# Optimization experiments

Measured on AMD Instinct MI355X. Metric: run time of the kernel, lower is better.

Reference implementation:

```python
import jax, jax.numpy as jnp
from jax import lax
import numpy as np

B, A, D = 4, 512, 729   # batch, num_angles, detector pixels
H, W = 512, 512         # reconstruction volume


def setup_inputs() -> dict:
    key = jax.random.key(0)
    sino = jax.random.normal(key, (B, A, D), dtype=jnp.float32)
    vol_spacing = np.array([1.0, 1.0], dtype=np.float32)          # (sy, sx)
    det_spacing = np.array([1.0], dtype=np.float32)
    vol_origin = np.array([-(H - 1) / 2.0, -(W - 1) / 2.0], dtype=np.float32)
    det_origin = np.array([-(D - 1) / 2.0], dtype=np.float32)
    angles = jnp.linspace(0.0, jnp.pi, A, endpoint=False, dtype=jnp.float32)
    return {
        "input": sino,
        "volume_shape": np.array([H, W], dtype=np.int64),
        "volume_origin": jnp.asarray(vol_origin),
        "detector_origin": jnp.asarray(det_origin),
        "volume_spacing": jnpp if False else jnp.asarray(vol_spacing),
        "detector_spacing": jnp.asarray(det_spacing),
        "trajectory": angles,
    }


def _backproject(sino, vol_shape, vol_origin, det_origin, vol_spacing, det_spacing, angles):
    h, w = int(vol_shape[0]), int(vol_shape[1])
    d = sino.shape[-1]
    ys = vol_origin[0] + jnp.arange(h, dtype=sino.dtype) * vol_spacing[0]  # [H]
    xs = vol_origin[1] + jnp.arange(w, dtype=sino.dtype) * vol_spacing[1]  # [W]

    def step(acc, per_angle):
        theta, sino_a = per_angle                      # scalar, [B, D]
        # ray coordinate s = x*cos(theta) + y*sin(theta) for every voxel
        s = xs[None, :] * jnp.cos(theta) + ys[:, None] * jnp.sin(theta)  # [H, W]
        u = (s - det_origin[0]) / det_spacing[0]       # continuous detector index
        u0 = jnp.floor(u)
        frac = u - u0
        i0 = u0.astype(jnp.int32)
        i1 = i0 + 1
        valid0 = (i0 >= 0) & (i0 < d)
        valid1 = (i1 >= 0) & (i1 < d)
        i0c = jnp.clip(i0, 0, d - 1)
        i1c = jnp.clip(i1, 0, d - 1)
        v0 = sino_a[:, i0c]                            # [B, H, W] gather
        v1 = sino_a[:, i1c]                            # [B, H, W] gather
        contrib = (jnp.where(valid0, (1.0 - frac) * v0, 0.0)
                   + jnp.where(valid1, frac * v1, 0.0))
        return acc + contrib, None

    acc0 = jnp.zeros((sino.shape[0], h, w), dtype=sino.dtype)
    out, _ = lax.scan(step, acc0, (angles, jnp.swapaxes(sino, 0, 1)))
    return out


def reference(input, volume_shape, volume_origin, detector_origin,
              volume_spacing, detector_spacing, trajectory):
    return _backproject(input, volume_shape, volume_origin, detector_origin,
                        volume_spacing, detector_spacing, trajectory)
```

## Files before the change

kernel.cpp:

```cpp
#include <hip/hip_runtime.h>

#define BB 4
#define AA 512
#define ZS 8
#define AH (AA / ZS)
#define DD 729
#define HH 512
#define WW 512
#define CH 4
#define NC (AH / CH)
#define WIN 32

typedef float f4v __attribute__((ext_vector_type(4)));

__device__ inline void gload_lds(const float* g, float* l) {
    __builtin_amdgcn_global_load_lds(
        (const __attribute__((address_space(1))) unsigned int*)g,
        (__attribute__((address_space(3))) unsigned int*)l, 4, 0, 0);
}

#define WAIT_VM8 0x0F78
#define WAIT_VM0 0x0F70

__global__ __launch_bounds__(64, 8) void bp_kernel(
    const float* __restrict__ sino,
    const float* __restrict__ vol_origin,
    const float* __restrict__ det_origin,
    const float* __restrict__ vol_spacing,
    const float* __restrict__ det_spacing,
    const float* __restrict__ angles,
    float* __restrict__ out)
{
    __shared__ f4v   s_csk[AH];
    __shared__ int   s_s0[AH];
    __shared__ float s_win[2][CH * WIN * BB];

    const int lane = threadIdx.y * 16 + threadIdx.x;

    const float inv_ds = 1.0f / det_spacing[0];
    const int abase = blockIdx.z * AH;

    const int x0 = blockIdx.x * 16;
    const int y0 = blockIdx.y * 16;
    const float vsx = vol_spacing[1], vsy = vol_spacing[0];
    const float off = -det_origin[0] * inv_ds;
    const float xc = vol_origin[1] + ((float)x0 + 7.5f) * vsx;
    const float yc = vol_origin[0] + ((float)y0 + 7.5f) * vsy;

    {
        const int a = lane;
        float th = angles[abase + a];
        float c = cosf(th) * inv_ds;
        float s = sinf(th) * inv_ds;
        float uc = fmaf(xc, c, fmaf(yc, s, off));
        int s0 = min(max((int)uc - (WIN / 2), 0), DD - WIN);
        f4v k;
        k.x = c; k.y = s; k.z = off - (float)s0; k.w = 4.0f * vsy * s;
        s_csk[a] = k;
        s_s0[a]  = s0;
    }
    __builtin_amdgcn_s_waitcnt(0xC070);

    const int ix  = x0 + threadIdx.x;
    const int iy0 = y0 + threadIdx.y;
    const float xw = vol_origin[1] + (float)ix * vsx;
    const float yw = vol_origin[0] + (float)iy0 * vsy;

    const long sg0 = (long)(lane & 3) * (AA * DD) + (lane >> 2);

    f4v acc0 = {0.f, 0.f, 0.f, 0.f};
    f4v acc1 = {0.f, 0.f, 0.f, 0.f};
    f4v acc2 = {0.f, 0.f, 0.f, 0.f};
    f4v acc3 = {0.f, 0.f, 0.f, 0.f};

    #define STAGE(C, P)                                                    \
        do {                                                               \
            _Pragma("unroll")                                              \
            for (int i = 0; i < CH; ++i) {                                 \
                const int  aa  = (C) * CH + i;                             \
                const long row = (long)(abase + aa) * DD + s_s0[aa];       \
                float* dst = &s_win[P][i * (WIN * BB)];                    \
                gload_lds(sino + row + sg0, dst);                          \
                gload_lds(sino + row + sg0 + 16, dst + 64);                \
            }                                                              \
        } while (0)

    #define LERP(U, ACC)                                                   \
        do {                                                               \
            const int   li = (int)(U);                                     \
            const float fr = __builtin_amdgcn_fractf(U);                   \
            const float om = 1.0f - fr;                                    \
            const f4v* w = (const f4v*)&s_win[p][(j * WIN + li) * BB];     \
            const f4v P = w[0], Q = w[1];                                  \
            const f4v fr4 = {fr, fr, fr, fr};                              \
            const f4v om4 = {om, om, om, om};                              \
            ACC = ACC + fr4 * Q + om4 * P;                                 \
        } while (0)

    int p = 0;
    STAGE(0, 0);
    for (int c = 0; c < NC; ++c) {
        if (c + 1 < NC) {
            STAGE(c + 1, p ^ 1);
            __builtin_amdgcn_s_waitcnt(WAIT_VM8);
        } else {
            __builtin_amdgcn_s_waitcnt(WAIT_VM0);
        }
        #pragma unroll
        for (int j = 0; j < CH; ++j) {
            const f4v  k  = s_csk[c * CH + j];
            const float u0 = fmaf(xw, k.x, fmaf(yw, k.y, k.z));
            const float u1 = u0 + k.w;
            const float u2 = u1 + k.w;
            const float u3 = u2 + k.w;
            LERP(u0, acc0);
            LERP(u1, acc1);
            LERP(u2, acc2);
            LERP(u3, acc3);
        }
        p ^= 1;
    }
    #undef STAGE
    #undef LERP

    const size_t HW = (size_t)HH * WW;
    #define OUT4(ACC, ROWOFF)                                              \
        do {                                                               \
            const size_t o = (size_t)(iy0 + (ROWOFF)) * WW + ix;           \
            unsafeAtomicAdd(&out[o],          (ACC).x);                    \
            unsafeAtomicAdd(&out[o + HW],     (ACC).y);                    \
            unsafeAtomicAdd(&out[o + 2 * HW], (ACC).z);                    \
            unsafeAtomicAdd(&out[o + 3 * HW], (ACC).w);                    \
        } while (0)
    OUT4(acc0, 0);
    OUT4(acc1, 4);
    OUT4(acc2, 8);
    OUT4(acc3, 12);
    #undef OUT4
}

extern "C" void kernel_launch(void* const* d_in, const int* in_sizes, int n_in,
                              void* d_out, int out_size, void* d_ws, size_t ws_size,
                              hipStream_t stream) {
    const float* sino        = (const float*)d_in[0];
    const float* vol_origin  = (const float*)d_in[2];
    const float* det_origin  = (const float*)d_in[3];
    const float* vol_spacing = (const float*)d_in[4];
    const float* det_spacing = (const float*)d_in[5];
    const float* angles      = (const float*)d_in[6];
    float* out = (float*)d_out;

    hipMemsetAsync(d_out, 0, (size_t)out_size * sizeof(float), stream);

    dim3 block(16, 4, 1);
    dim3 grid(WW / 16, HH / 16, ZS);
    bp_kernel<<<grid, block, 0, stream>>>(sino, vol_origin, det_origin,
                                          vol_spacing, det_spacing, angles, out);
}
```

Measured before the change: 139.7 us.

## Stage sinogram windows as packed fp16 and interpolate with half2 FMAs

Replaces the direct global-to-LDS double-buffered staging with buffer loads into registers. The loaded values are converted to packed fp16 pairs and written to a single LDS buffer between two barriers. Interpolation then runs with half2 FMAs, and the fp16 partial sums are widened into fp32 accumulators after every chunk of four angles. This halves LDS footprint and read bandwidth and doubles arithmetic density, but adds two barriers per chunk, conversion work, and fp16 precision loss. It also lowers the occupancy hint in the launch bounds.

```diff
diff --git a/kernel.cpp b/kernel.cpp
--- a/kernel.cpp
+++ b/kernel.cpp
@@ -1,4 +1,5 @@
 #include <hip/hip_runtime.h>
+#include <hip/hip_fp16.h>
 
 #define BB 4
 #define AA 512
@@ -11,18 +12,22 @@
 #define NC (AH / CH)
 #define WIN 32
 
-typedef float f4v __attribute__((ext_vector_type(4)));
+typedef float        f4v  __attribute__((ext_vector_type(4)));
+typedef unsigned int u4v8 __attribute__((ext_vector_type(4), aligned(8)));
 
-__device__ inline void gload_lds(const float* g, float* l) {
-    __builtin_amdgcn_global_load_lds(
-        (const __attribute__((address_space(1))) unsigned int*)g,
-        (__attribute__((address_space(3))) unsigned int*)l, 4, 0, 0);
+__device__ inline float buf_load1(__amdgpu_buffer_rsrc_t r, int elem) {
+    union { unsigned int u; float f; } c;
+    c.u = __builtin_amdgcn_raw_buffer_load_b32(r, elem * 4, 0, 0);
+    return c.f;
+}
+__device__ inline __half2 h2bc(unsigned int x) {
+    return __builtin_bit_cast(__half2, x);
+}
+__device__ inline unsigned int pk2u(float a, float b) {
+    return __builtin_bit_cast(unsigned int, __builtin_amdgcn_cvt_pkrtz(a, b));
 }
 
-#define WAIT_VM8 0x0F78
-#define WAIT_VM0 0x0F70
-
-__global__ __launch_bounds__(64, 8) void bp_kernel(
+__global__ __launch_bounds__(64, 4) void bp_kernel(
     const float* __restrict__ sino,
     const float* __restrict__ vol_origin,
     const float* __restrict__ det_origin,
@@ -31,9 +36,9 @@
     const float* __restrict__ angles,
     float* __restrict__ out)
 {
-    __shared__ f4v   s_csk[AH];
-    __shared__ int   s_s0[AH];
-    __shared__ float s_win[2][CH * WIN * BB];
+    __shared__ f4v          s_csk[AH];
+    __shared__ int          s_s0[AH];
+    __shared__ unsigned int s_win[CH * WIN * 2];
 
     const int lane = threadIdx.y * 16 + threadIdx.x;
 
@@ -59,53 +64,76 @@
         s_csk[a] = k;
         s_s0[a]  = s0;
     }
-    __builtin_amdgcn_s_waitcnt(0xC070);
+    __syncthreads();
 
     const int ix  = x0 + threadIdx.x;
     const int iy0 = y0 + threadIdx.y;
     const float xw = vol_origin[1] + (float)ix * vsx;
     const float yw = vol_origin[0] + (float)iy0 * vsy;
 
-    const long sg0 = (long)(lane & 3) * (AA * DD) + (lane >> 2);
+    const int hh = lane & 1;
+    const int ee = lane >> 1;
+    const int gA = (2 * hh) * (AA * DD) + ee;
+
+    const __amdgpu_buffer_rsrc_t rsrc = __builtin_amdgcn_make_buffer_rsrc(
+        (void*)sino, (short)0, BB * AA * DD * 4, 0x00020000);
 
     f4v acc0 = {0.f, 0.f, 0.f, 0.f};
     f4v acc1 = {0.f, 0.f, 0.f, 0.f};
     f4v acc2 = {0.f, 0.f, 0.f, 0.f};
     f4v acc3 = {0.f, 0.f, 0.f, 0.f};
 
-    #define STAGE(C, P)                                                    \
+    const __half2 hz = h2bc(0u);
+    __half2 h01_0 = hz, h23_0 = hz, h01_1 = hz, h23_1 = hz;
+    __half2 h01_2 = hz, h23_2 = hz, h01_3 = hz, h23_3 = hz;
+
+    float vA0, vB0, vA1, vB1, vA2, vB2, vA3, vB3;
+
+    #define STAGE_LOAD(C)                                                  \
         do {                                                               \
-            _Pragma("unroll")                                              \
-            for (int i = 0; i < CH; ++i) {                                 \
-                const int  aa  = (C) * CH + i;                             \
-                const long row = (long)(abase + aa) * DD + s_s0[aa];       \
-                float* dst = &s_win[P][i * (WIN * BB)];                    \
-                gload_lds(sino + row + sg0, dst);                          \
-                gload_lds(sino + row + sg0 + 16, dst + 64);                \
-            }                                                              \
+            const int aa = (C) * CH;                                       \
+            const int r0 = (abase + aa + 0) * DD + s_s0[aa + 0] + gA;      \
+            const int r1 = (abase + aa + 1) * DD + s_s0[aa + 1] + gA;      \
+            const int r2 = (abase + aa + 2) * DD + s_s0[aa + 2] + gA;      \
+            const int r3 = (abase + aa + 3) * DD + s_s0[aa + 3] + gA;      \
+            vA0 = buf_load1(rsrc, r0); vB0 = buf_load1(rsrc, r0 + AA * DD);\
+            vA1 = buf_load1(rsrc, r1); vB1 = buf_load1(rsrc, r1 + AA * DD);\
+            vA2 = buf_load1(rsrc, r2); vB2 = buf_load1(rsrc, r2 + AA * DD);\
+            vA3 = buf_load1(rsrc, r3); vB3 = buf_load1(rsrc, r3 + AA * DD);\
         } while (0)
 
-    #define LERP(U, ACC)                                                   \
+    #define CONVERT_WRITE()                                                \
+        do {                                                               \
+            s_win[0 * 64 + lane] = pk2u(vA0, vB0);                         \
+            s_win[1 * 64 + lane] = pk2u(vA1, vB1);                         \
+            s_win[2 * 64 + lane] = pk2u(vA2, vB2);                         \
+            s_win[3 * 64 + lane] = pk2u(vA3, vB3);                         \
+        } while (0)
+
+    #define LERP(U, H01, H23)                                              \
         do {                                                               \
             const int   li = (int)(U);                                     \
             const float fr = __builtin_amdgcn_fractf(U);                   \
-            const float om = 1.0f - fr;                                    \
-            const f4v* w = (const f4v*)&s_win[p][(j * WIN + li) * BB];     \
-            const f4v P = w[0], Q = w[1];                                  \
-            const f4v fr4 = {fr, fr, fr, fr};                              \
-            const f4v om4 = {om, om, om, om};                              \
-            ACC = ACC + fr4 * Q + om4 * P;                                 \
+            const __half2 fr2 = h2bc(pk2u(fr, fr));                        \
+            const __half2 om2 = h2bc(pk2u(1.0f - fr, 1.0f - fr));          \
+            const u4v8 t = *(const u4v8*)&s_win[(j * WIN + li) * 2];       \
+            H01 = __hfma2(h2bc(t.x), om2, __hfma2(h2bc(t.z), fr2, H01));   \
+            H23 = __hfma2(h2bc(t.y), om2, __hfma2(h2bc(t.w), fr2, H23));   \
         } while (0)
 
-    int p = 0;
-    STAGE(0, 0);
+    #define WIDEN(H01, H23, ACC)                                           \
+        do {                                                               \
+            (ACC).x += __low2float(H01);  (ACC).y += __high2float(H01);    \
+            (ACC).z += __low2float(H23);  (ACC).w += __high2float(H23);    \
+            H01 = hz; H23 = hz;                                            \
+        } while (0)
+
+    STAGE_LOAD(0);
     for (int c = 0; c < NC; ++c) {
-        if (c + 1 < NC) {
-            STAGE(c + 1, p ^ 1);
-            __builtin_amdgcn_s_waitcnt(WAIT_VM8);
-        } else {
-            __builtin_amdgcn_s_waitcnt(WAIT_VM0);
-        }
+        __syncthreads();
+        CONVERT_WRITE();
+        __syncthreads();
+        if (c + 1 < NC) STAGE_LOAD(c + 1);
         #pragma unroll
         for (int j = 0; j < CH; ++j) {
             const f4v  k  = s_csk[c * CH + j];
@@ -113,15 +141,20 @@
             const float u1 = u0 + k.w;
             const float u2 = u1 + k.w;
             const float u3 = u2 + k.w;
-            LERP(u0, acc0);
-            LERP(u1, acc1);
-            LERP(u2, acc2);
-            LERP(u3, acc3);
+            LERP(u0, h01_0, h23_0);
+            LERP(u1, h01_1, h23_1);
+            LERP(u2, h01_2, h23_2);
+            LERP(u3, h01_3, h23_3);
         }
-        p ^= 1;
+        WIDEN(h01_0, h23_0, acc0);
+        WIDEN(h01_1, h23_1, acc1);
+        WIDEN(h01_2, h23_2, acc2);
+        WIDEN(h01_3, h23_3, acc3);
     }
-    #undef STAGE
+    #undef STAGE_LOAD
+    #undef CONVERT_WRITE
     #undef LERP
+    #undef WIDEN
 
     const size_t HW = (size_t)HH * WW;
     #define OUT4(ACC, ROWOFF)                                              \
```

Result: faster. 123.4 us (-11.7%).
